# Optimization experiments

Hardware: AMD Instinct MI355X
Metric: run time of the kernel (lower is better)

## Reference

```python
import jax, jax.numpy as jnp
import numpy as np


def setup_inputs() -> dict:
    key = jax.random.key(0)
    ks = jax.random.split(key, 7)
    N, D, K = 500000, 128, 32
    return {
        "x": jax.random.normal(ks[0], (N, D), dtype=jnp.float32),
        "h_e": jax.random.normal(ks[1], (N, D), dtype=jnp.float32),
        "bond_n": jax.random.uniform(ks[2], (K, N), dtype=jnp.float32),
        "W_i_w": jax.random.normal(ks[3], (D, 2 * D), dtype=jnp.float32) * 0.05,
        "W_i_b": jax.random.normal(ks[4], (D,), dtype=jnp.float32) * 0.05,
        "W_m_w": jax.random.normal(ks[5], (D, D), dtype=jnp.float32) * 0.05,
        "W_m_b": jax.random.normal(ks[6], (D,), dtype=jnp.float32) * 0.05,
    }


def reference(x, h_e, bond_n, W_i_w, W_i_b, W_m_w, W_m_b):
    # h_n = relu(W_i([x ; h_e]))  -> [N, D]
    h_n = jax.nn.relu(jnp.concatenate([x, h_e], axis=1) @ W_i_w.T + W_i_b)
    # m = sum_k sum_n bond_n[k,n] * h_n[n,:]  -> [D]
    # (equivalent to torch: (bond_n[...,None] * h_n).sum(1).sum(0),
    #  but expressed as a contraction to avoid the [K,N,D] intermediate)
    m = jnp.einsum('kn,nd->d', bond_n, h_n)
    # h = relu(h_n + W_m(m))  -> [N, D] via broadcast of the [D] message
    h = jax.nn.relu(h_n + (m @ W_m_w.T + W_m_b))
    return h
```

## Files before the change

### kernel.cpp

```cpp
#include <hip/hip_runtime.h>
#include <stdint.h>
#include <stddef.h>

#define N_ROWS 500000
#define DDIM   128
#define K2     256
#define KBOND  32
#define TILE_ROWS 64
#define NT ((N_ROWS + TILE_ROWS - 1) / TILE_ROWS)
#define NB1 2048
#define P2_BLOCKS 2048

typedef float  f32x4  __attribute__((ext_vector_type(4)));
typedef __bf16 bf16x8 __attribute__((ext_vector_type(8)));
typedef __bf16 bf16x4 __attribute__((ext_vector_type(4)));

__device__ __bf16 g_wbf[DDIM * K2];
__device__ float  g_partials[NB1 * DDIM];
__device__ float  g_m[DDIM];
__device__ float  g_msg[DDIM];
__device__ __bf16 g_hn[(size_t)N_ROWS * DDIM];

__global__ void k_prep(const float* __restrict__ w) {
  int t = blockIdx.x * blockDim.x + threadIdx.x;
  if (t < DDIM * K2) g_wbf[t] = (__bf16)w[t];
}

__global__ __launch_bounds__(512)
void k_pass1(const float* __restrict__ x, const float* __restrict__ he,
             const float* __restrict__ bond, const float* __restrict__ bias)
{
  __shared__ __align__(16) unsigned char a_lds[TILE_ROWS * 512];
  __shared__ float s_lds[TILE_ROWS];
  __shared__ float mred[DDIM];

  const int tid  = threadIdx.x;
  const int w    = tid >> 6;
  const int lane = tid & 63;
  const int l15  = lane & 15;
  const int g    = lane >> 4;

  bf16x8 wfrag[8];
  #pragma unroll
  for (int ks = 0; ks < 8; ++ks)
    wfrag[ks] = *(const bf16x8*)(g_wbf + (size_t)(16 * w + l15) * K2 + ks * 32 + 8 * g);

  const int d0 = 16 * w + 4 * g;
  const f32x4 bv = *(const f32x4*)(bias + d0);

  f32x4 macc = (f32x4)(0.f);

  for (int tile = blockIdx.x; tile < NT; tile += gridDim.x) {
    const int rb_blk = tile * TILE_ROWS;

    #pragma unroll
    for (int it = 0; it < 4; ++it) {
      const int r  = it * 16 + (tid >> 5);
      const int k4 = (tid & 31) * 4;
      int n  = rb_blk + r;
      int nc = n < N_ROWS ? n : (N_ROWS - 1);
      f32x4 xv = *(const f32x4*)(x  + (size_t)nc * DDIM + k4);
      f32x4 hv = *(const f32x4*)(he + (size_t)nc * DDIM + k4);
      bf16x4 xb, hb;
      #pragma unroll
      for (int i = 0; i < 4; ++i) { xb[i] = (__bf16)xv[i]; hb[i] = (__bf16)hv[i]; }
      const int sw = (r & 7) << 4;
      *(bf16x4*)(a_lds + r * 512 + ((2 * k4) ^ sw))         = xb;
      *(bf16x4*)(a_lds + r * 512 + ((2 * (128 + k4)) ^ sw)) = hb;
    }

    if (tid < TILE_ROWS) {
      int n = rb_blk + tid;
      float s = 0.f;
      if (n < N_ROWS) {
        #pragma unroll
        for (int k = 0; k < KBOND; ++k) s += bond[(size_t)k * N_ROWS + n];
      }
      s_lds[tid] = s;
    }
    __syncthreads();

    f32x4 acc[4];
    #pragma unroll
    for (int i = 0; i < 4; ++i) acc[i] = (f32x4)(0.f);

    #pragma unroll
    for (int ks = 0; ks < 8; ++ks) {
      bf16x8 bfrag[4];
      #pragma unroll
      for (int nf = 0; nf < 4; ++nf) {
        const int r = 16 * nf + l15;
        bfrag[nf] = *(const bf16x8*)(a_lds + r * 512 +
                                     ((64 * ks + 16 * g) ^ ((r & 7) << 4)));
      }
      #pragma unroll
      for (int nf = 0; nf < 4; ++nf)
        acc[nf] = __builtin_amdgcn_mfma_f32_16x16x32_bf16(wfrag[ks], bfrag[nf],
                                                          acc[nf], 0, 0, 0);
    }

    #pragma unroll
    for (int nf = 0; nf < 4; ++nf) {
      const int lr = 16 * nf + l15;
      const int n  = rb_blk + lr;
      const float sn = s_lds[lr];
      f32x4 h;
      #pragma unroll
      for (int i = 0; i < 4; ++i) {
        float v = acc[nf][i] + bv[i];
        h[i] = v > 0.f ? v : 0.f;
      }
      macc += sn * h;
      if (n < N_ROWS) {
        bf16x4 hb;
        #pragma unroll
        for (int i = 0; i < 4; ++i) hb[i] = (__bf16)h[i];
        *(bf16x4*)(g_hn + (size_t)n * DDIM + d0) = hb;
      }
    }
    __syncthreads();
  }

  #pragma unroll
  for (int off = 1; off <= 8; off <<= 1) {
    #pragma unroll
    for (int i = 0; i < 4; ++i) macc[i] += __shfl_xor(macc[i], off, 64);
  }
  if (l15 == 0) {
    #pragma unroll
    for (int i = 0; i < 4; ++i) mred[d0 + i] = macc[i];
  }
  __syncthreads();
  if (tid < DDIM)
    g_partials[(size_t)blockIdx.x * DDIM + tid] = mred[tid];
}

__global__ void k_mreduce() {
  const int d = blockIdx.x;
  float s = 0.f;
  for (int i = threadIdx.x; i < NB1; i += 256) s += g_partials[(size_t)i * DDIM + d];
  #pragma unroll
  for (int off = 32; off >= 1; off >>= 1) s += __shfl_down(s, off, 64);
  __shared__ float red[4];
  if ((threadIdx.x & 63) == 0) red[threadIdx.x >> 6] = s;
  __syncthreads();
  if (threadIdx.x == 0) g_m[d] = red[0] + red[1] + red[2] + red[3];
}

__global__ void k_msg(const float* __restrict__ wm, const float* __restrict__ bm) {
  __shared__ float ms[DDIM];
  if (threadIdx.x < DDIM) ms[threadIdx.x] = g_m[threadIdx.x];
  __syncthreads();
  const int d = threadIdx.x;
  if (d < DDIM) {
    float acc = bm[d];
    #pragma unroll 8
    for (int j = 0; j < DDIM; ++j) acc += ms[j] * wm[(size_t)d * DDIM + j];
    g_msg[d] = acc;
  }
}

__global__ __launch_bounds__(256)
void k_pass2(float* __restrict__ out)
{
  __shared__ float ms[DDIM];
  if (threadIdx.x < DDIM) ms[threadIdx.x] = g_msg[threadIdx.x];
  __syncthreads();
  const size_t total = (size_t)N_ROWS * DDIM / 8;
  for (size_t c = (size_t)blockIdx.x * blockDim.x + threadIdx.x; c < total;
       c += (size_t)gridDim.x * blockDim.x) {
    const size_t base = c * 8;
    const int col0 = (int)(base & (DDIM - 1));
    bf16x8 hv = *(const bf16x8*)(g_hn + base);
    f32x4 o0, o1;
    #pragma unroll
    for (int i = 0; i < 4; ++i) {
      float a = (float)hv[i]     + ms[col0 + i];
      float b = (float)hv[4 + i] + ms[col0 + 4 + i];
      o0[i] = a > 0.f ? a : 0.f;
      o1[i] = b > 0.f ? b : 0.f;
    }
    *(f32x4*)(out + base)     = o0;
    *(f32x4*)(out + base + 4) = o1;
  }
}

extern "C" void kernel_launch(void* const* d_in, const int* in_sizes, int n_in,
                              void* d_out, int out_size, void* d_ws, size_t ws_size,
                              hipStream_t stream) {
  const float* x    = (const float*)d_in[0];
  const float* he   = (const float*)d_in[1];
  const float* bond = (const float*)d_in[2];
  const float* wi   = (const float*)d_in[3];
  const float* bi   = (const float*)d_in[4];
  const float* wm   = (const float*)d_in[5];
  const float* bm   = (const float*)d_in[6];
  float* out = (float*)d_out;
  (void)d_ws; (void)ws_size;

  k_prep<<<(DDIM * K2 + 255) / 256, 256, 0, stream>>>(wi);
  k_pass1<<<NB1, 512, 0, stream>>>(x, he, bond, bi);
  k_mreduce<<<DDIM, 256, 0, stream>>>();
  k_msg<<<1, 128, 0, stream>>>(wm, bm);
  k_pass2<<<P2_BLOCKS, 256, 0, stream>>>(out);
}
```

Baseline: 255.0 us.

## Launch one pass1 block per tile and restructure the message reduction

Pass 1 changes from a persistent 2048-block grid-stride loop to one block per 64-row tile (about 7800 blocks). The goal is more in-flight memory requests and no serialized loop per block. The bond row-sum is split across all 8 waves with an LDS reduction instead of 64 threads each doing 32 strided loads. Input staging uses 16-byte bf16x8 LDS stores with a 16-way swizzle. The column reduction becomes two stages over the larger partials array, which adds a little extra partial-sum traffic.

```diff
diff --git a/kernel.cpp b/kernel.cpp
--- a/kernel.cpp
+++ b/kernel.cpp
@@ -8,7 +8,8 @@
 #define KBOND  32
 #define TILE_ROWS 64
 #define NT ((N_ROWS + TILE_ROWS - 1) / TILE_ROWS)
-#define NB1 2048
+#define MR_CH 64
+#define NCH ((NT + MR_CH - 1) / MR_CH)
 #define P2_BLOCKS 2048
 
 typedef float  f32x4  __attribute__((ext_vector_type(4)));
@@ -16,8 +17,8 @@
 typedef __bf16 bf16x4 __attribute__((ext_vector_type(4)));
 
 __device__ __bf16 g_wbf[DDIM * K2];
-__device__ float  g_partials[NB1 * DDIM];
-__device__ float  g_m[DDIM];
+__device__ float  g_partials[(size_t)NT * DDIM];
+__device__ float  g_p2[NCH * DDIM];
 __device__ float  g_msg[DDIM];
 __device__ __bf16 g_hn[(size_t)N_ROWS * DDIM];
 
@@ -31,14 +32,15 @@
              const float* __restrict__ bond, const float* __restrict__ bias)
 {
   __shared__ __align__(16) unsigned char a_lds[TILE_ROWS * 512];
+  __shared__ float s_part[8][TILE_ROWS];
   __shared__ float s_lds[TILE_ROWS];
-  __shared__ float mred[DDIM];
 
   const int tid  = threadIdx.x;
   const int w    = tid >> 6;
   const int lane = tid & 63;
   const int l15  = lane & 15;
   const int g    = lane >> 4;
+  const int rb   = blockIdx.x * TILE_ROWS;
 
   bf16x8 wfrag[8];
   #pragma unroll
@@ -48,77 +50,80 @@
   const int d0 = 16 * w + 4 * g;
   const f32x4 bv = *(const f32x4*)(bias + d0);
 
+  #pragma unroll
+  for (int it = 0; it < 4; ++it) {
+    const int r = ((it & 1) ? 32 : 0) + (tid >> 4);
+    const int c = tid & 15;
+    const float* src = (it < 2) ? x : he;
+    int n  = rb + r;
+    int nc = n < N_ROWS ? n : (N_ROWS - 1);
+    f32x4 v0 = *(const f32x4*)(src + (size_t)nc * DDIM + 8 * c);
+    f32x4 v1 = *(const f32x4*)(src + (size_t)nc * DDIM + 8 * c + 4);
+    bf16x8 b;
+    #pragma unroll
+    for (int i = 0; i < 4; ++i) { b[i] = (__bf16)v0[i]; b[4 + i] = (__bf16)v1[i]; }
+    const int base = (it < 2) ? 0 : 256;
+    *(bf16x8*)(a_lds + r * 512 + ((base + 16 * c) ^ ((r & 15) << 4))) = b;
+  }
+
+  {
+    const int row = tid & 63, kg = tid >> 6;
+    int n = rb + row;
+    float p = 0.f;
+    if (n < N_ROWS) {
+      #pragma unroll
+      for (int j = 0; j < 4; ++j) p += bond[(size_t)(4 * kg + j) * N_ROWS + n];
+    }
+    s_part[kg][row] = p;
+  }
+  __syncthreads();
+
+  if (tid < TILE_ROWS) {
+    float s = 0.f;
+    #pragma unroll
+    for (int kg = 0; kg < 8; ++kg) s += s_part[kg][tid];
+    s_lds[tid] = s;
+  }
+
+  f32x4 acc[4];
+  #pragma unroll
+  for (int i = 0; i < 4; ++i) acc[i] = (f32x4)(0.f);
+
+  #pragma unroll
+  for (int ks = 0; ks < 8; ++ks) {
+    bf16x8 bfrag[4];
+    #pragma unroll
+    for (int nf = 0; nf < 4; ++nf) {
+      const int r = 16 * nf + l15;
+      bfrag[nf] = *(const bf16x8*)(a_lds + r * 512 +
+                                   ((64 * ks + 16 * g) ^ ((r & 15) << 4)));
+    }
+    #pragma unroll
+    for (int nf = 0; nf < 4; ++nf)
+      acc[nf] = __builtin_amdgcn_mfma_f32_16x16x32_bf16(wfrag[ks], bfrag[nf],
+                                                        acc[nf], 0, 0, 0);
+  }
+  __syncthreads();
+
   f32x4 macc = (f32x4)(0.f);
-
-  for (int tile = blockIdx.x; tile < NT; tile += gridDim.x) {
-    const int rb_blk = tile * TILE_ROWS;
-
-    #pragma unroll
-    for (int it = 0; it < 4; ++it) {
-      const int r  = it * 16 + (tid >> 5);
-      const int k4 = (tid & 31) * 4;
-      int n  = rb_blk + r;
-      int nc = n < N_ROWS ? n : (N_ROWS - 1);
-      f32x4 xv = *(const f32x4*)(x  + (size_t)nc * DDIM + k4);
-      f32x4 hv = *(const f32x4*)(he + (size_t)nc * DDIM + k4);
-      bf16x4 xb, hb;
+  #pragma unroll
+  for (int nf = 0; nf < 4; ++nf) {
+    const int lr = 16 * nf + l15;
+    const int n  = rb + lr;
+    const float sn = s_lds[lr];
+    f32x4 h;
+    #pragma unroll
+    for (int i = 0; i < 4; ++i) {
+      float v = acc[nf][i] + bv[i];
+      h[i] = v > 0.f ? v : 0.f;
+    }
+    macc += sn * h;
+    if (n < N_ROWS) {
+      bf16x4 hb;
       #pragma unroll
-      for (int i = 0; i < 4; ++i) { xb[i] = (__bf16)xv[i]; hb[i] = (__bf16)hv[i]; }
-      const int sw = (r & 7) << 4;
-      *(bf16x4*)(a_lds + r * 512 + ((2 * k4) ^ sw))         = xb;
-      *(bf16x4*)(a_lds + r * 512 + ((2 * (128 + k4)) ^ sw)) = hb;
-    }
-
-    if (tid < TILE_ROWS) {
-      int n = rb_blk + tid;
-      float s = 0.f;
-      if (n < N_ROWS) {
-        #pragma unroll
-        for (int k = 0; k < KBOND; ++k) s += bond[(size_t)k * N_ROWS + n];
-      }
-      s_lds[tid] = s;
-    }
-    __syncthreads();
-
-    f32x4 acc[4];
-    #pragma unroll
-    for (int i = 0; i < 4; ++i) acc[i] = (f32x4)(0.f);
-
-    #pragma unroll
-    for (int ks = 0; ks < 8; ++ks) {
-      bf16x8 bfrag[4];
-      #pragma unroll
-      for (int nf = 0; nf < 4; ++nf) {
-        const int r = 16 * nf + l15;
-        bfrag[nf] = *(const bf16x8*)(a_lds + r * 512 +
-                                     ((64 * ks + 16 * g) ^ ((r & 7) << 4)));
-      }
-      #pragma unroll
-      for (int nf = 0; nf < 4; ++nf)
-        acc[nf] = __builtin_amdgcn_mfma_f32_16x16x32_bf16(wfrag[ks], bfrag[nf],
-                                                          acc[nf], 0, 0, 0);
-    }
-
-    #pragma unroll
-    for (int nf = 0; nf < 4; ++nf) {
-      const int lr = 16 * nf + l15;
-      const int n  = rb_blk + lr;
-      const float sn = s_lds[lr];
-      f32x4 h;
-      #pragma unroll
-      for (int i = 0; i < 4; ++i) {
-        float v = acc[nf][i] + bv[i];
-        h[i] = v > 0.f ? v : 0.f;
-      }
-      macc += sn * h;
-      if (n < N_ROWS) {
-        bf16x4 hb;
-        #pragma unroll
-        for (int i = 0; i < 4; ++i) hb[i] = (__bf16)h[i];
-        *(bf16x4*)(g_hn + (size_t)n * DDIM + d0) = hb;
-      }
-    }
-    __syncthreads();
+      for (int i = 0; i < 4; ++i) hb[i] = (__bf16)h[i];
+      *(bf16x4*)(g_hn + (size_t)n * DDIM + d0) = hb;
+    }
   }
 
   #pragma unroll
@@ -126,38 +131,36 @@
     #pragma unroll
     for (int i = 0; i < 4; ++i) macc[i] += __shfl_xor(macc[i], off, 64);
   }
-  if (l15 == 0) {
-    #pragma unroll
-    for (int i = 0; i < 4; ++i) mred[d0 + i] = macc[i];
-  }
-  __syncthreads();
-  if (tid < DDIM)
-    g_partials[(size_t)blockIdx.x * DDIM + tid] = mred[tid];
-}
-
-__global__ void k_mreduce() {
-  const int d = blockIdx.x;
-  float s = 0.f;
-  for (int i = threadIdx.x; i < NB1; i += 256) s += g_partials[(size_t)i * DDIM + d];
-  #pragma unroll
-  for (int off = 32; off >= 1; off >>= 1) s += __shfl_down(s, off, 64);
-  __shared__ float red[4];
-  if ((threadIdx.x & 63) == 0) red[threadIdx.x >> 6] = s;
-  __syncthreads();
-  if (threadIdx.x == 0) g_m[d] = red[0] + red[1] + red[2] + red[3];
+  if (l15 == 0)
+    *(f32x4*)(&g_partials[(size_t)blockIdx.x * DDIM + d0]) = macc;
+}
+
+__global__ void k_mr1() {
+  const int c  = blockIdx.x;
+  const int r0 = c * MR_CH;
+  const int d    = threadIdx.x & 127;
+  const int half = threadIdx.x >> 7;
+  const int rend = (r0 + MR_CH < NT) ? (r0 + MR_CH) : NT;
+  float acc = 0.f;
+  for (int r = r0 + half; r < rend; r += 2)
+    acc += g_partials[(size_t)r * DDIM + d];
+  __shared__ float sp[DDIM];
+  if (half == 0) sp[d] = acc;
+  __syncthreads();
+  if (half == 1) g_p2[c * DDIM + d] = sp[d] + acc;
 }
 
 __global__ void k_msg(const float* __restrict__ wm, const float* __restrict__ bm) {
   __shared__ float ms[DDIM];
-  if (threadIdx.x < DDIM) ms[threadIdx.x] = g_m[threadIdx.x];
-  __syncthreads();
   const int d = threadIdx.x;
-  if (d < DDIM) {
-    float acc = bm[d];
-    #pragma unroll 8
-    for (int j = 0; j < DDIM; ++j) acc += ms[j] * wm[(size_t)d * DDIM + j];
-    g_msg[d] = acc;
-  }
+  float s = 0.f;
+  for (int c = 0; c < NCH; ++c) s += g_p2[c * DDIM + d];
+  ms[d] = s;
+  __syncthreads();
+  float acc = bm[d];
+  #pragma unroll 8
+  for (int j = 0; j < DDIM; ++j) acc += ms[j] * wm[(size_t)d * DDIM + j];
+  g_msg[d] = acc;
 }
 
 __global__ __launch_bounds__(256)
@@ -199,8 +202,8 @@
   (void)d_ws; (void)ws_size;
 
   k_prep<<<(DDIM * K2 + 255) / 256, 256, 0, stream>>>(wi);
-  k_pass1<<<NB1, 512, 0, stream>>>(x, he, bond, bi);
-  k_mreduce<<<DDIM, 256, 0, stream>>>();
+  k_pass1<<<NT, 512, 0, stream>>>(x, he, bond, bi);
+  k_mr1<<<NCH, 256, 0, stream>>>();
   k_msg<<<1, 128, 0, stream>>>(wm, bm);
   k_pass2<<<P2_BLOCKS, 256, 0, stream>>>(out);
 }
```

Measured after the change: 284.8 us. 11.7% more time.
